# Optimization experiments

Measured on AMD Instinct MI355X. Metric: run time of the kernel, lower is better.

The kernel has to match this reference:

```python
import jax, jax.numpy as jnp
from jax import lax
import numpy as np

MAX_ITER = 12      # sifting iterations per IMF
TOL = 0.05         # sd tolerance / flatness tolerance
NUM_IMFS = 6       # max IMFs extracted
EPS = 1e-8


def _peak_mask(s):
    # strict local maxima, matching scipy.signal.find_peaks on plateau-free
    # (continuous random) signals: s[i-1] < s[i] > s[i+1]
    interior = (s[:, 1:-1] > s[:, :-2]) & (s[:, 1:-1] > s[:, 2:])
    return jnp.pad(interior, ((0, 0), (1, 1)))  # [B, L] bool


def _interp_env(s, mask):
    # piecewise-linear interpolation through masked peaks, flat extrapolation
    # at the ends (np.interp with left=first peak val, right=last peak val)
    B, L = s.shape
    idx = jnp.arange(L)
    last = lax.cummax(jnp.where(mask, idx, -1), axis=1)               # prev peak idx (-1 if none)
    nxt = lax.cummin(jnp.where(mask, idx, L), axis=1, reverse=True)   # next peak idx (L if none)
    vl = jnp.take_along_axis(s, jnp.clip(last, 0, L - 1), axis=1)
    vr = jnp.take_along_axis(s, jnp.clip(nxt, 0, L - 1), axis=1)
    denom = nxt - last
    frac = jnp.where(denom > 0,
                     (idx - last).astype(s.dtype) / jnp.maximum(denom, 1).astype(s.dtype),
                     jnp.zeros((), s.dtype))
    env = vl + frac * (vr - vl)
    env = jnp.where(last < 0, vr, env)   # left of first peak
    env = jnp.where(nxt >= L, vl, env)   # right of last peak
    return env


def _envelope(s, upper):
    mask = _peak_mask(s) if upper else _peak_mask(-s)
    env = _interp_env(s, mask)
    # fallback when fewer than 2 peaks: running max / running min of s
    fb = lax.cummax(s, axis=1) if upper else lax.cummin(s, axis=1)
    few = mask.sum(axis=1, keepdims=True) < 2
    return jnp.where(few, fb, env)


def _extract_imf(signal):
    # iterative sifting with early-stop masked into a fixed-length scan
    def body(carry, _):
        h, done = carry
        mean = 0.5 * (_envelope(h, True) + _envelope(h, False))
        # sd = sum((h - h_new)^2) / (sum(h^2)+eps) and h - h_new == mean
        sd = jnp.sum(mean ** 2) / (jnp.sum(h ** 2) + EPS)
        conv = sd < TOL
        h_next = jnp.where(done | conv, h, h - mean)
        return (h_next, done | conv), None
    (h, _), _ = lax.scan(body, (signal, jnp.array(False)), None, length=MAX_ITER)
    return h, signal - h


def _emd(x):
    def step(carry, _):
        res, done = carry
        imf, new_res = _extract_imf(res)
        imf = jnp.where(done, jnp.zeros_like(imf), imf)
        new_res = jnp.where(done, res, new_res)
        # _is_residual_flat: var(diff) < tol * var(residual) (torch.var unbiased)
        d = jnp.diff(new_res, axis=-1)
        flat = jnp.var(d, ddof=1) < TOL * jnp.var(new_res, ddof=1)
        return (new_res, done | flat), imf
    (res, _), imfs = lax.scan(step, (x, jnp.array(False)), None, length=NUM_IMFS)
    # stack IMFs and residual: [NUM_IMFS+1, B, L]; IMFs after early stop are zeros
    return jnp.concatenate([imfs, res[None]], axis=0)


def setup_inputs() -> dict:
    key = jax.random.key(0)
    x = jax.random.normal(key, (64, 16384), dtype=jnp.float32)
    return {"x": x}


def reference(x):
    return _emd(x)
```

## Files before the change

kernel.cpp:

```cpp
#include <hip/hip_runtime.h>

#define NL 16384
#define NB 64
#define NT 1024
#define NC (NL / NT)
#define NW (NT / 64)
#define N_ITER 12
#define N_IMFS 6

#pragma clang fp contract(off)

#define HSZ (NL + (NL >> 5))
__device__ __forceinline__ int physi(int i) { return i + (i >> 5); }

#define FMAXV 3.402823466e38f

__global__ __launch_bounds__(NT, 4) void emd_main(
    const float* __restrict__ x, float* __restrict__ out,
    unsigned* cnt, double* sdsl, double* flsl) {
  __shared__ float hbuf[2 * HSZ];
  __shared__ int wLU[NW], wLL[NW], wNU[NW], wNL[NW];
  __shared__ float wMx[NW], wMn[NW];
  __shared__ unsigned wCT[NW];
  __shared__ int eLU[NW], eLL[NW], eNU[NW], eNL[NW];
  __shared__ float eMx[NW], eMn[NW];
  __shared__ unsigned sTot;
  __shared__ double tA[NW], tB[NW], tC[NW], tD[NW];
  __shared__ int sFlag;

  const int t = threadIdx.x;
  const int lane = t & 63;
  const int wv = t >> 6;
  const int row = blockIdx.x;
  const int base = t * NC;
  const float* xr = x + (size_t)row * NL;
  float* res = out + (size_t)N_IMFS * NB * NL + (size_t)row * NL;

  int off = 0;

  #pragma unroll
  for (int q = 0; q < NC / 4; q++) {
    int i0 = base + q * 4;
    float4 v = *(const float4*)&xr[i0];
    *(float4*)&hbuf[physi(i0)] = v;
    *(float4*)&res[i0] = v;
  }
  __syncthreads();

  unsigned ep = 0;
  bool done = false;

  for (int k = 0; k < N_IMFS; k++) {
    float* outk = out + (size_t)k * NB * NL + (size_t)row * NL;
    if (done) {
      #pragma unroll
      for (int q = 0; q < NC / 4; q++)
        *(float4*)&outk[base + q * 4] = make_float4(0.f, 0.f, 0.f, 0.f);
      continue;
    }

    for (int it = 0; it < N_ITER; it++) {
      float* hcur = hbuf + off;
      float* hnx  = hbuf + (off ^ HSZ);

      unsigned mU = 0, mL = 0;
      int lmU = -1, lmL = -1, cU = 0, cL = 0;
      float rmx = -FMAXV, rmn = FMAXV;
      {
        float hm = (base > 0) ? hcur[physi(base - 1)] : 0.0f;
        float4 cur = *(const float4*)&hcur[physi(base)];
        #define PKSTEP(J, HC, HP) { int i = base + (J);                     \
          bool in = (i > 0) && (i + 1 < NL);                                \
          if (in && hm < (HC) && (HC) > (HP)) { mU |= 1u << (J); lmU = i; cU++; } \
          if (in && hm > (HC) && (HC) < (HP)) { mL |= 1u << (J); lmL = i; cL++; } \
          rmx = fmaxf(rmx, (HC)); rmn = fminf(rmn, (HC)); hm = (HC); }
        #pragma unroll
        for (int q = 0; q < 4; q++) {
          float4 nxt = cur;
          float n0;
          if (q < 3) { nxt = *(const float4*)&hcur[physi(base + q * 4 + 4)]; n0 = nxt.x; }
          else       { n0 = (base + 16 < NL) ? hcur[physi(base + 16)] : 0.0f; }
          PKSTEP(q * 4 + 0, cur.x, cur.y)
          PKSTEP(q * 4 + 1, cur.y, cur.z)
          PKSTEP(q * 4 + 2, cur.z, cur.w)
          PKSTEP(q * 4 + 3, cur.w, n0)
          cur = nxt;
        }
        #undef PKSTEP
      }
      int fpU = mU ? (base + __ffs(mU) - 1) : NL;
      int fpL = mL ? (base + __ffs(mL) - 1) : NL;
      unsigned long long bUm = __ballot(mU != 0);
      unsigned long long bLm = __ballot(mL != 0);
      {
        int s;
        s = bUm ? (63 - __clzll((long long)bUm)) : 0;
        if (lane == s) wLU[wv] = bUm ? lmU : -1;
        s = bLm ? (63 - __clzll((long long)bLm)) : 0;
        if (lane == s) wLL[wv] = bLm ? lmL : -1;
        s = bUm ? (__ffsll(bUm) - 1) : 0;
        if (lane == s) wNU[wv] = bUm ? fpU : NL;
        s = bLm ? (__ffsll(bLm) - 1) : 0;
        if (lane == s) wNL[wv] = bLm ? fpL : NL;
      }
      unsigned ict = ((unsigned)cU << 16) | (unsigned)cL;
      #pragma unroll
      for (int o = 1; o < 64; o <<= 1) {
        unsigned cc = __shfl_down(ict, o, 64);
        if (lane + o < 64) ict += cc;
      }
      if (lane == 0) wCT[wv] = ict;
      __syncthreads();
      if (t == 0) {
        int aLU = -1, aLL = -1; unsigned tt = 0;
        for (int w = 0; w < NW; w++) {
          eLU[w] = aLU; aLU = max(aLU, wLU[w]);
          eLL[w] = aLL; aLL = max(aLL, wLL[w]);
          tt += wCT[w];
        }
        int aNU = NL, aNL = NL;
        for (int w = NW - 1; w >= 0; w--) {
          eNU[w] = aNU; aNU = min(aNU, wNU[w]);
          eNL[w] = aNL; aNL = min(aNL, wNL[w]);
        }
        sTot = tt;
      }
      __syncthreads();
      const unsigned tot = sTot;
      const int totU = (int)(tot >> 16), totL = (int)(tot & 0xffffu);

      unsigned long long belowU = bUm & ((1ull << lane) - 1ull);
      unsigned long long belowL = bLm & ((1ull << lane) - 1ull);
      unsigned long long aboveU = (lane == 63) ? 0ull : (bUm & (~0ull << (lane + 1)));
      unsigned long long aboveL = (lane == 63) ? 0ull : (bLm & (~0ull << (lane + 1)));
      int slU = belowU ? (63 - __clzll((long long)belowU)) : 0;
      int slL = belowL ? (63 - __clzll((long long)belowL)) : 0;
      int snU = aboveU ? (__ffsll(aboveU) - 1) : 0;
      int snL = aboveL ? (__ffsll(aboveL) - 1) : 0;
      int gU  = __shfl(lmU, slU, 64);
      int gL  = __shfl(lmL, slL, 64);
      int gNU = __shfl(fpU, snU, 64);
      int gNL = __shfl(fpL, snL, 64);
      const int clU = belowU ? gU  : eLU[wv];
      const int clL = belowL ? gL  : eLL[wv];
      const int cnU = aboveU ? gNU : eNU[wv];
      const int cnL = aboveL ? gNL : eNL[wv];

      float crx = -FMAXV, crn = FMAXV;
      if (totU < 2 || totL < 2) {
        float iMx = rmx, iMn = rmn;
        #pragma unroll
        for (int o = 1; o < 64; o <<= 1) {
          float fa = __shfl_up(iMx, o, 64);
          float fb = __shfl_up(iMn, o, 64);
          if (lane >= o) { iMx = fmaxf(iMx, fa); iMn = fminf(iMn, fb); }
        }
        if (lane == 63) { wMx[wv] = iMx; wMn[wv] = iMn; }
        __syncthreads();
        if (t == 0) {
          float aMx = -FMAXV, aMn = FMAXV;
          for (int w = 0; w < NW; w++) {
            eMx[w] = aMx; aMx = fmaxf(aMx, wMx[w]);
            eMn[w] = aMn; aMn = fminf(aMn, wMn[w]);
          }
        }
        __syncthreads();
        float pMx = __shfl_up(iMx, 1, 64); if (lane == 0) pMx = -FMAXV;
        float pMn = __shfl_up(iMn, 1, 64); if (lane == 0) pMn = FMAXV;
        crx = fmaxf(eMx[wv], pMx);
        crn = fminf(eMn[wv], pMn);
      }

      double pm2 = 0.0, ph2 = 0.0;
      {
        float rx = crx, rn = crn;
        int curLU = clU, curLL = clL;
        float vl = hcur[physi(clU < 0 ? 0 : clU)];
        float wl = hcur[physi(clL < 0 ? 0 : clL)];
        int gB = -0x7fffffff, gD = -0x7fffffff;
        float vr = 0.0f, wr = 0.0f;
        #define ENVSTEP(J, HC, OD) { int i = base + (J); float hc = (HC);   \
          rx = fmaxf(rx, hc); rn = fminf(rn, hc);                           \
          if ((mU >> (J)) & 1u) { curLU = i; vl = hc; }                     \
          if ((mL >> (J)) & 1u) { curLL = i; wl = hc; }                     \
          int lU = curLU, lL = curLL;                                       \
          unsigned highm = 0xFFFFFFFFu << (J); unsigned a;                  \
          a = mU & highm; int nUv = a ? (base + __ffs(a) - 1) : cnU;        \
          a = mL & highm; int nLv = a ? (base + __ffs(a) - 1) : cnL;        \
          if (nUv != gB) { gB = nUv; vr = hcur[physi(nUv >= NL ? NL - 1 : nUv)]; } \
          if (nLv != gD) { gD = nLv; wr = hcur[physi(nLv >= NL ? NL - 1 : nLv)]; } \
          int den = nUv - lU;                                               \
          float fracU = (float)(i - lU) / (float)(den > 0 ? den : 1);       \
          float envU = (den > 0) ? __builtin_fmaf(fracU, vr - vl, vl) : vl; \
          if (lU < 0) envU = vr;                                            \
          if (nUv >= NL) envU = vl;                                         \
          if (totU < 2) envU = rx;                                          \
          int den2 = nLv - lL;                                              \
          float fracL = (float)(i - lL) / (float)(den2 > 0 ? den2 : 1);     \
          float envL = (den2 > 0) ? __builtin_fmaf(fracL, wr - wl, wl) : wl;\
          if (lL < 0) envL = wr;                                            \
          if (nLv >= NL) envL = wl;                                         \
          if (totL < 2) envL = rn;                                          \
          float mn = 0.5f * (envU + envL);                                  \
          (OD) = hc - mn;                                                   \
          pm2 += (double)mn * (double)mn; ph2 += (double)hc * (double)hc; }
        #pragma unroll
        for (int q = 0; q < 4; q++) {
          int i0 = base + q * 4;
          float4 hv4 = *(const float4*)&hcur[physi(i0)];
          float4 o4;
          ENVSTEP(q * 4 + 0, hv4.x, o4.x)
          ENVSTEP(q * 4 + 1, hv4.y, o4.y)
          ENVSTEP(q * 4 + 2, hv4.z, o4.z)
          ENVSTEP(q * 4 + 3, hv4.w, o4.w)
          *(float4*)&hnx[physi(i0)] = o4;
        }
        #undef ENVSTEP
      }
      #pragma unroll
      for (int o = 1; o < 64; o <<= 1) {
        double a = __shfl_down(pm2, o, 64);
        double b = __shfl_down(ph2, o, 64);
        if (lane + o < 64) { pm2 += a; ph2 += b; }
      }
      if (lane == 0) { tA[wv] = pm2; tB[wv] = ph2; }
      ep++;
      __syncthreads();
      if (t == 0) {
        double sA = 0.0, sB = 0.0;
        for (int w = 0; w < NW; w++) { sA += tA[w]; sB += tB[w]; }
        atomicAdd(&sdsl[(k * N_ITER + it) * 2 + 0], sA);
        atomicAdd(&sdsl[(k * N_ITER + it) * 2 + 1], sB);
        __hip_atomic_fetch_add(cnt, 1u, __ATOMIC_ACQ_REL, __HIP_MEMORY_SCOPE_AGENT);
        unsigned tgt = ep * gridDim.x;
        while (__hip_atomic_load(cnt, __ATOMIC_ACQUIRE, __HIP_MEMORY_SCOPE_AGENT) < tgt)
          __builtin_amdgcn_s_sleep(1);
        double m2 = __hip_atomic_load(&sdsl[(k * N_ITER + it) * 2 + 0],
                                      __ATOMIC_RELAXED, __HIP_MEMORY_SCOPE_AGENT);
        double h2 = __hip_atomic_load(&sdsl[(k * N_ITER + it) * 2 + 1],
                                      __ATOMIC_RELAXED, __HIP_MEMORY_SCOPE_AGENT);
        sFlag = (m2 / (h2 + 1e-8) < 0.05) ? 1 : 0;
      }
      __syncthreads();
      if (sFlag) break;
      off ^= HSZ;
    }

    float* hcur = hbuf + off;
    double s1 = 0.0, s2 = 0.0, s3 = 0.0, s4 = 0.0;
    {
      float rb = 0.0f;
      if (base + NC < NL) rb = res[base + NC] - hcur[physi(base + NC)];
      float4 rv4 = *(const float4*)&res[base];
      float4 hv4 = *(const float4*)&hcur[physi(base)];
      float e0 = rv4.x - hv4.x, e1 = rv4.y - hv4.y,
            e2 = rv4.z - hv4.z, e3 = rv4.w - hv4.w;
      #define FLSTEP(J, CUR, NXT) { int i = base + (J);                     \
        s1 += (double)(CUR); s2 += (double)(CUR) * (double)(CUR);           \
        if (i + 1 < NL) { float dd = (NXT) - (CUR);                         \
          s3 += (double)dd; s4 += (double)dd * (double)dd; } }
      #pragma unroll
      for (int q = 0; q < 4; q++) {
        float c0 = e0, c1 = e1, c2 = e2, c3 = e3;
        float n0;
        if (q < 3) {
          int i0 = base + q * 4 + 4;
          rv4 = *(const float4*)&res[i0];
          hv4 = *(const float4*)&hcur[physi(i0)];
          e0 = rv4.x - hv4.x; e1 = rv4.y - hv4.y;
          e2 = rv4.z - hv4.z; e3 = rv4.w - hv4.w;
          n0 = e0;
        } else n0 = rb;
        FLSTEP(q * 4 + 0, c0, c1)
        FLSTEP(q * 4 + 1, c1, c2)
        FLSTEP(q * 4 + 2, c2, c3)
        FLSTEP(q * 4 + 3, c3, n0)
      }
      #undef FLSTEP
    }
    #pragma unroll
    for (int o = 1; o < 64; o <<= 1) {
      double a = __shfl_down(s1, o, 64);
      double b = __shfl_down(s2, o, 64);
      double c = __shfl_down(s3, o, 64);
      double d = __shfl_down(s4, o, 64);
      if (lane + o < 64) { s1 += a; s2 += b; s3 += c; s4 += d; }
    }
    if (lane == 0) { tA[wv] = s1; tB[wv] = s2; tC[wv] = s3; tD[wv] = s4; }
    __syncthreads();
    if (t == 0) {
      double S1 = 0.0, S2 = 0.0, S3 = 0.0, S4 = 0.0;
      for (int w = 0; w < NW; w++) { S1 += tA[w]; S2 += tB[w]; S3 += tC[w]; S4 += tD[w]; }
      atomicAdd(&flsl[k * 4 + 0], S1);
      atomicAdd(&flsl[k * 4 + 1], S2);
      atomicAdd(&flsl[k * 4 + 2], S3);
      atomicAdd(&flsl[k * 4 + 3], S4);
    }
    #pragma unroll
    for (int q = 0; q < NC / 4; q++) {
      int i0 = base + q * 4;
      int p0 = physi(i0);
      float4 rv = *(const float4*)&res[i0];
      float4 hv = *(const float4*)&hcur[p0];
      float4 rq = make_float4(rv.x - hv.x, rv.y - hv.y, rv.z - hv.z, rv.w - hv.w);
      *(float4*)&outk[i0] = hv;
      *(float4*)&res[i0] = rq;
      *(float4*)&hcur[p0] = rq;
    }
    ep++;
    __syncthreads();
    if (t == 0) {
      __hip_atomic_fetch_add(cnt, 1u, __ATOMIC_ACQ_REL, __HIP_MEMORY_SCOPE_AGENT);
      unsigned tgt = ep * gridDim.x;
      while (__hip_atomic_load(cnt, __ATOMIC_ACQUIRE, __HIP_MEMORY_SCOPE_AGENT) < tgt)
        __builtin_amdgcn_s_sleep(1);
      double S1 = __hip_atomic_load(&flsl[k * 4 + 0], __ATOMIC_RELAXED, __HIP_MEMORY_SCOPE_AGENT);
      double S2 = __hip_atomic_load(&flsl[k * 4 + 1], __ATOMIC_RELAXED, __HIP_MEMORY_SCOPE_AGENT);
      double S3 = __hip_atomic_load(&flsl[k * 4 + 2], __ATOMIC_RELAXED, __HIP_MEMORY_SCOPE_AGENT);
      double S4 = __hip_atomic_load(&flsl[k * 4 + 3], __ATOMIC_RELAXED, __HIP_MEMORY_SCOPE_AGENT);
      double nr = (double)NB * (double)NL;
      double nd = (double)NB * (double)(NL - 1);
      double varr = (S2 - S1 * S1 / nr) / (nr - 1.0);
      double vard = (S4 - S3 * S3 / nd) / (nd - 1.0);
      sFlag = (vard < 0.05 * varr) ? 1 : 0;
    }
    __syncthreads();
    done = done || (sFlag != 0);
  }
}

extern "C" void kernel_launch(void* const* d_in, const int* in_sizes, int n_in,
                              void* d_out, int out_size, void* d_ws, size_t ws_size,
                              hipStream_t stream) {
  const float* x = (const float*)d_in[0];
  float* out = (float*)d_out;
  size_t zb = ws_size < 4096 ? ws_size : 4096;
  hipMemsetAsync(d_ws, 0, zb, stream);
  unsigned* cnt = (unsigned*)d_ws;
  double* sdsl = (double*)((char*)d_ws + 256);
  double* flsl = (double*)((char*)d_ws + 256 + (size_t)N_IMFS * N_ITER * 2 * 8);
  hipLaunchKernelGGL(emd_main, dim3(NB), dim3(NT), 0, stream, x, out, cnt, sdsl, flsl);
}
```

Before: 286.2 us.

## Split each row across four cooperating blocks with global boundary exchange

Each signal row is now handled by four blocks, one per quarter-segment, so the grid grows from 64 to 256 blocks and each thread owns 4 samples instead of 16. Blocks of the same row trade boundary samples, per-segment peak summaries and running max/min through workspace memory, and wait on a per-row atomic counter barrier every sifting iteration. The aim is to occupy more compute units, since 64 blocks leave most of the GPU idle. The cost is an extra inter-block spin barrier and global-memory round trips on every iteration.

```diff
diff --git a/kernel.cpp b/kernel.cpp
--- a/kernel.cpp
+++ b/kernel.cpp
@@ -2,94 +2,124 @@
 
 #define NL 16384
 #define NB 64
+#define NSEG 4
+#define SEG (NL / NSEG)
 #define NT 1024
-#define NC (NL / NT)
+#define NC (SEG / NT)
 #define NW (NT / 64)
 #define N_ITER 12
 #define N_IMFS 6
 
 #pragma clang fp contract(off)
 
-#define HSZ (NL + (NL >> 5))
+#define HSZS (SEG + (SEG >> 5))
 __device__ __forceinline__ int physi(int i) { return i + (i >> 5); }
 
 #define FMAXV 3.402823466e38f
 
+__device__ __forceinline__ void gstore(float* p, float v) {
+  __hip_atomic_store(p, v, __ATOMIC_RELAXED, __HIP_MEMORY_SCOPE_AGENT);
+}
+__device__ __forceinline__ float gload(float* p) {
+  return __hip_atomic_load(p, __ATOMIC_RELAXED, __HIP_MEMORY_SCOPE_AGENT);
+}
+
 __global__ __launch_bounds__(NT, 4) void emd_main(
-    const float* __restrict__ x, float* __restrict__ out,
-    unsigned* cnt, double* sdsl, double* flsl) {
-  __shared__ float hbuf[2 * HSZ];
+    const float* __restrict__ x, float* __restrict__ out, char* __restrict__ ws) {
+  unsigned* cnt    = (unsigned*)ws;
+  double*   sdsl   = (double*)(ws + 256);
+  double*   flsl   = (double*)(ws + 1408);
+  unsigned* rowcnt = (unsigned*)(ws + 2048);
+  float*    hbg    = (float*)(ws + 6144);
+  float*    bsm    = (float*)(ws + 10240);
+  float*    rsb    = (float*)(ws + 26624);
+
+  __shared__ float hbuf[2 * HSZS];
   __shared__ int wLU[NW], wLL[NW], wNU[NW], wNL[NW];
   __shared__ float wMx[NW], wMn[NW];
   __shared__ unsigned wCT[NW];
   __shared__ int eLU[NW], eLL[NW], eNU[NW], eNL[NW];
+  __shared__ float eLUv[NW], eLLv[NW], eNUv[NW], eNLv[NW];
   __shared__ float eMx[NW], eMn[NW];
+  __shared__ float bsl[12];
+  __shared__ float nbs[NSEG][12];
   __shared__ unsigned sTot;
+  __shared__ float sBMx, sBMn;
   __shared__ double tA[NW], tB[NW], tC[NW], tD[NW];
   __shared__ int sFlag;
 
   const int t = threadIdx.x;
   const int lane = t & 63;
   const int wv = t >> 6;
-  const int row = blockIdx.x;
-  const int base = t * NC;
+  const int bid = blockIdx.x;
+  const int row = bid >> 2;
+  const int seg = bid & 3;
+  const int seg0 = seg * SEG;
+  const int seg1 = seg0 + SEG;
+  const int bl = t * NC;
+  const int bg = seg0 + bl;
   const float* xr = x + (size_t)row * NL;
   float* res = out + (size_t)N_IMFS * NB * NL + (size_t)row * NL;
 
   int off = 0;
-
-  #pragma unroll
-  for (int q = 0; q < NC / 4; q++) {
-    int i0 = base + q * 4;
-    float4 v = *(const float4*)&xr[i0];
-    *(float4*)&hbuf[physi(i0)] = v;
-    *(float4*)&res[i0] = v;
+  int hb = 0;
+  unsigned ep = 0;
+  unsigned rep = 0;
+
+  {
+    float4 v = *(const float4*)&xr[bg];
+    *(float4*)&hbuf[physi(bl)] = v;
+    *(float4*)&res[bg] = v;
+    if (t == 0) { gstore(&hbg[(0 * 256 + bid) * 2 + 0], v.x); gstore(&rsb[bid], v.x); }
+    if (t == NT - 1) gstore(&hbg[(0 * 256 + bid) * 2 + 1], v.w);
   }
   __syncthreads();
-
-  unsigned ep = 0;
+  rep++;
+  if (t == 0) {
+    __hip_atomic_fetch_add(&rowcnt[row * 16], 1u, __ATOMIC_ACQ_REL, __HIP_MEMORY_SCOPE_AGENT);
+    while (__hip_atomic_load(&rowcnt[row * 16], __ATOMIC_ACQUIRE, __HIP_MEMORY_SCOPE_AGENT) < rep * NSEG)
+      __builtin_amdgcn_s_sleep(1);
+  }
+  __syncthreads();
+
   bool done = false;
 
   for (int k = 0; k < N_IMFS; k++) {
     float* outk = out + (size_t)k * NB * NL + (size_t)row * NL;
     if (done) {
-      #pragma unroll
-      for (int q = 0; q < NC / 4; q++)
-        *(float4*)&outk[base + q * 4] = make_float4(0.f, 0.f, 0.f, 0.f);
+      *(float4*)&outk[bg] = make_float4(0.f, 0.f, 0.f, 0.f);
       continue;
     }
 
     for (int it = 0; it < N_ITER; it++) {
       float* hcur = hbuf + off;
-      float* hnx  = hbuf + (off ^ HSZ);
+      float* hnx  = hbuf + (off ^ HSZS);
 
       unsigned mU = 0, mL = 0;
       int lmU = -1, lmL = -1, cU = 0, cL = 0;
       float rmx = -FMAXV, rmn = FMAXV;
       {
-        float hm = (base > 0) ? hcur[physi(base - 1)] : 0.0f;
-        float4 cur = *(const float4*)&hcur[physi(base)];
-        #define PKSTEP(J, HC, HP) { int i = base + (J);                     \
-          bool in = (i > 0) && (i + 1 < NL);                                \
+        float hbPrev = 0.0f, hbNext = 0.0f;
+        if (bl == 0 && bg > 0)
+          hbPrev = gload(&hbg[(hb * 256 + bid - 1) * 2 + 1]);
+        if (bl + NC == SEG && bg + NC < NL)
+          hbNext = gload(&hbg[(hb * 256 + bid + 1) * 2 + 0]);
+        float hm = (bg > 0) ? ((bl > 0) ? hcur[physi(bl - 1)] : hbPrev) : 0.0f;
+        float nextv = (bl + NC < SEG) ? hcur[physi(bl + NC)] : hbNext;
+        float4 cur = *(const float4*)&hcur[physi(bl)];
+        #define PKSTEP(J, HC, HP) { int i = bg + (J);                         \
+          bool in = (i > 0) && (i + 1 < NL);                                  \
           if (in && hm < (HC) && (HC) > (HP)) { mU |= 1u << (J); lmU = i; cU++; } \
           if (in && hm > (HC) && (HC) < (HP)) { mL |= 1u << (J); lmL = i; cL++; } \
           rmx = fmaxf(rmx, (HC)); rmn = fminf(rmn, (HC)); hm = (HC); }
-        #pragma unroll
-        for (int q = 0; q < 4; q++) {
-          float4 nxt = cur;
-          float n0;
-          if (q < 3) { nxt = *(const float4*)&hcur[physi(base + q * 4 + 4)]; n0 = nxt.x; }
-          else       { n0 = (base + 16 < NL) ? hcur[physi(base + 16)] : 0.0f; }
-          PKSTEP(q * 4 + 0, cur.x, cur.y)
-          PKSTEP(q * 4 + 1, cur.y, cur.z)
-          PKSTEP(q * 4 + 2, cur.z, cur.w)
-          PKSTEP(q * 4 + 3, cur.w, n0)
-          cur = nxt;
-        }
+        PKSTEP(0, cur.x, cur.y)
+        PKSTEP(1, cur.y, cur.z)
+        PKSTEP(2, cur.z, cur.w)
+        PKSTEP(3, cur.w, nextv)
         #undef PKSTEP
       }
-      int fpU = mU ? (base + __ffs(mU) - 1) : NL;
-      int fpL = mL ? (base + __ffs(mL) - 1) : NL;
+      int fpU = mU ? (bg + __ffs(mU) - 1) : NL;
+      int fpL = mL ? (bg + __ffs(mL) - 1) : NL;
       unsigned long long bUm = __ballot(mU != 0);
       unsigned long long bLm = __ballot(mL != 0);
       {
@@ -104,26 +134,89 @@
         if (lane == s) wNL[wv] = bLm ? fpL : NL;
       }
       unsigned ict = ((unsigned)cU << 16) | (unsigned)cL;
-      #pragma unroll
-      for (int o = 1; o < 64; o <<= 1) {
-        unsigned cc = __shfl_down(ict, o, 64);
-        if (lane + o < 64) ict += cc;
-      }
-      if (lane == 0) wCT[wv] = ict;
+      {
+        float wmx = rmx, wmn = rmn;
+        #pragma unroll
+        for (int o = 1; o < 64; o <<= 1) {
+          unsigned cc = __shfl_down(ict, o, 64);
+          float fa = __shfl_down(wmx, o, 64);
+          float fb = __shfl_down(wmn, o, 64);
+          if (lane + o < 64) { ict += cc; wmx = fmaxf(wmx, fa); wmn = fminf(wmn, fb); }
+        }
+        if (lane == 0) { wCT[wv] = ict; wMx[wv] = wmx; wMn[wv] = wmn; }
+      }
       __syncthreads();
       if (t == 0) {
-        int aLU = -1, aLL = -1; unsigned tt = 0;
+        int aLU = -1, aLL = -1, aNU = NL, aNL = NL;
+        float aMx = -FMAXV, aMn = FMAXV; unsigned tt = 0;
         for (int w = 0; w < NW; w++) {
-          eLU[w] = aLU; aLU = max(aLU, wLU[w]);
-          eLL[w] = aLL; aLL = max(aLL, wLL[w]);
+          if (wLU[w] > aLU) aLU = wLU[w];
+          if (wLL[w] > aLL) aLL = wLL[w];
+          if (wNU[w] < aNU) aNU = wNU[w];
+          if (wNL[w] < aNL) aNL = wNL[w];
+          aMx = fmaxf(aMx, wMx[w]); aMn = fminf(aMn, wMn[w]);
           tt += wCT[w];
         }
-        int aNU = NL, aNL = NL;
+        bsl[0] = __int_as_float(aLU);
+        bsl[1] = (aLU >= 0) ? hcur[physi(aLU - seg0)] : 0.0f;
+        bsl[2] = __int_as_float(aLL);
+        bsl[3] = (aLL >= 0) ? hcur[physi(aLL - seg0)] : 0.0f;
+        bsl[4] = __int_as_float(aNU);
+        bsl[5] = (aNU < NL) ? hcur[physi(aNU - seg0)] : 0.0f;
+        bsl[6] = __int_as_float(aNL);
+        bsl[7] = (aNL < NL) ? hcur[physi(aNL - seg0)] : 0.0f;
+        bsl[8] = aMx; bsl[9] = aMn;
+        bsl[10] = __uint_as_float(tt);
+        bsl[11] = 0.f;
+      }
+      __syncthreads();
+      rep++;
+      if (wv == 0) {
+        if (lane < 12) gstore(&bsm[bid * 16 + lane], bsl[lane]);
+        if (lane == 0) {
+          __hip_atomic_fetch_add(&rowcnt[row * 16], 1u, __ATOMIC_ACQ_REL, __HIP_MEMORY_SCOPE_AGENT);
+          while (__hip_atomic_load(&rowcnt[row * 16], __ATOMIC_ACQUIRE, __HIP_MEMORY_SCOPE_AGENT) < rep * NSEG)
+            __builtin_amdgcn_s_sleep(1);
+        }
+        if (lane < 48) {
+          int s = lane / 12, sl = lane % 12;
+          nbs[s][sl] = gload(&bsm[(row * 4 + s) * 16 + sl]);
+        }
+      }
+      __syncthreads();
+      if (t == 0) {
+        int bclU = -1, bclL = -1; float bclUv = 0.f, bclLv = 0.f;
+        float bMx = -FMAXV, bMn = FMAXV;
+        for (int s = 0; s < seg; s++) {
+          int v = __float_as_int(nbs[s][0]);
+          if (v > bclU) { bclU = v; bclUv = nbs[s][1]; }
+          v = __float_as_int(nbs[s][2]);
+          if (v > bclL) { bclL = v; bclLv = nbs[s][3]; }
+          bMx = fmaxf(bMx, nbs[s][8]);
+          bMn = fminf(bMn, nbs[s][9]);
+        }
+        int bcnU = NL, bcnL = NL; float bcnUv = 0.f, bcnLv = 0.f;
+        for (int s = NSEG - 1; s > seg; s--) {
+          int v = __float_as_int(nbs[s][4]);
+          if (v < bcnU) { bcnU = v; bcnUv = nbs[s][5]; }
+          v = __float_as_int(nbs[s][6]);
+          if (v < bcnL) { bcnL = v; bcnLv = nbs[s][7]; }
+        }
+        unsigned tot = 0;
+        for (int s = 0; s < NSEG; s++) tot += __float_as_uint(nbs[s][10]);
+        sTot = tot; sBMx = bMx; sBMn = bMn;
+        int aLU = bclU, aLL = bclL; float aLUv = bclUv, aLLv = bclLv;
+        for (int w = 0; w < NW; w++) {
+          eLU[w] = aLU; eLUv[w] = aLUv; eLL[w] = aLL; eLLv[w] = aLLv;
+          if (wLU[w] > aLU) { aLU = wLU[w]; aLUv = hcur[physi(aLU - seg0)]; }
+          if (wLL[w] > aLL) { aLL = wLL[w]; aLLv = hcur[physi(aLL - seg0)]; }
+        }
+        int aNU = bcnU, aNL2 = bcnL; float aNUv = bcnUv, aNLv = bcnLv;
         for (int w = NW - 1; w >= 0; w--) {
-          eNU[w] = aNU; aNU = min(aNU, wNU[w]);
-          eNL[w] = aNL; aNL = min(aNL, wNL[w]);
-        }
-        sTot = tt;
+          eNU[w] = aNU; eNUv[w] = aNUv; eNL[w] = aNL2; eNLv[w] = aNLv;
+          if (wNU[w] < aNU) { aNU = wNU[w]; aNUv = hcur[physi(aNU - seg0)]; }
+          if (wNL[w] < aNL2) { aNL2 = wNL[w]; aNLv = hcur[physi(aNL2 - seg0)]; }
+        }
       }
       __syncthreads();
       const unsigned tot = sTot;
@@ -145,6 +238,10 @@
       const int clL = belowL ? gL  : eLL[wv];
       const int cnU = aboveU ? gNU : eNU[wv];
       const int cnL = aboveL ? gNL : eNL[wv];
+      const float cnUv = eNUv[wv];
+      const float cnLv = eNLv[wv];
+      float vl0 = belowU ? hcur[physi(gU - seg0)] : ((clU >= 0) ? eLUv[wv] : 0.0f);
+      float wl0 = belowL ? hcur[physi(gL - seg0)] : ((clL >= 0) ? eLLv[wv] : 0.0f);
 
       float crx = -FMAXV, crn = FMAXV;
       if (totU < 2 || totL < 2) {
@@ -158,7 +255,7 @@
         if (lane == 63) { wMx[wv] = iMx; wMn[wv] = iMn; }
         __syncthreads();
         if (t == 0) {
-          float aMx = -FMAXV, aMn = FMAXV;
+          float aMx = sBMx, aMn = sBMn;
           for (int w = 0; w < NW; w++) {
             eMx[w] = aMx; aMx = fmaxf(aMx, wMx[w]);
             eMn[w] = aMn; aMn = fminf(aMn, wMn[w]);
@@ -175,47 +272,47 @@
       {
         float rx = crx, rn = crn;
         int curLU = clU, curLL = clL;
-        float vl = hcur[physi(clU < 0 ? 0 : clU)];
-        float wl = hcur[physi(clL < 0 ? 0 : clL)];
+        float vl = vl0, wl = wl0;
         int gB = -0x7fffffff, gD = -0x7fffffff;
         float vr = 0.0f, wr = 0.0f;
-        #define ENVSTEP(J, HC, OD) { int i = base + (J); float hc = (HC);   \
-          rx = fmaxf(rx, hc); rn = fminf(rn, hc);                           \
-          if ((mU >> (J)) & 1u) { curLU = i; vl = hc; }                     \
-          if ((mL >> (J)) & 1u) { curLL = i; wl = hc; }                     \
-          int lU = curLU, lL = curLL;                                       \
-          unsigned highm = 0xFFFFFFFFu << (J); unsigned a;                  \
-          a = mU & highm; int nUv = a ? (base + __ffs(a) - 1) : cnU;        \
-          a = mL & highm; int nLv = a ? (base + __ffs(a) - 1) : cnL;        \
-          if (nUv != gB) { gB = nUv; vr = hcur[physi(nUv >= NL ? NL - 1 : nUv)]; } \
-          if (nLv != gD) { gD = nLv; wr = hcur[physi(nLv >= NL ? NL - 1 : nLv)]; } \
-          int den = nUv - lU;                                               \
-          float fracU = (float)(i - lU) / (float)(den > 0 ? den : 1);       \
-          float envU = (den > 0) ? __builtin_fmaf(fracU, vr - vl, vl) : vl; \
-          if (lU < 0) envU = vr;                                            \
-          if (nUv >= NL) envU = vl;                                         \
-          if (totU < 2) envU = rx;                                          \
-          int den2 = nLv - lL;                                              \
-          float fracL = (float)(i - lL) / (float)(den2 > 0 ? den2 : 1);     \
-          float envL = (den2 > 0) ? __builtin_fmaf(fracL, wr - wl, wl) : wl;\
-          if (lL < 0) envL = wr;                                            \
-          if (nLv >= NL) envL = wl;                                         \
-          if (totL < 2) envL = rn;                                          \
-          float mn = 0.5f * (envU + envL);                                  \
-          (OD) = hc - mn;                                                   \
+        #define ENVSTEP(J, HC, OD) { int i = bg + (J); float hc = (HC);       \
+          rx = fmaxf(rx, hc); rn = fminf(rn, hc);                             \
+          if ((mU >> (J)) & 1u) { curLU = i; vl = hc; }                       \
+          if ((mL >> (J)) & 1u) { curLL = i; wl = hc; }                       \
+          int lU = curLU, lL = curLL;                                         \
+          unsigned highm = 0xFFFFFFFFu << (J); unsigned a;                    \
+          a = mU & highm; int nUv = a ? (bg + __ffs(a) - 1) : cnU;            \
+          a = mL & highm; int nLv = a ? (bg + __ffs(a) - 1) : cnL;            \
+          if (nUv != gB) { gB = nUv;                                          \
+            vr = (nUv < seg1) ? hcur[physi(nUv - seg0)] : cnUv; }             \
+          if (nLv != gD) { gD = nLv;                                          \
+            wr = (nLv < seg1) ? hcur[physi(nLv - seg0)] : cnLv; }             \
+          int den = nUv - lU;                                                 \
+          float fracU = (float)(i - lU) / (float)(den > 0 ? den : 1);         \
+          float envU = (den > 0) ? __builtin_fmaf(fracU, vr - vl, vl) : vl;   \
+          if (lU < 0) envU = vr;                                              \
+          if (nUv >= NL) envU = vl;                                           \
+          if (totU < 2) envU = rx;                                            \
+          int den2 = nLv - lL;                                                \
+          float fracL = (float)(i - lL) / (float)(den2 > 0 ? den2 : 1);       \
+          float envL = (den2 > 0) ? __builtin_fmaf(fracL, wr - wl, wl) : wl;  \
+          if (lL < 0) envL = wr;                                              \
+          if (nLv >= NL) envL = wl;                                           \
+          if (totL < 2) envL = rn;                                            \
+          float mn = 0.5f * (envU + envL);                                    \
+          (OD) = hc - mn;                                                     \
           pm2 += (double)mn * (double)mn; ph2 += (double)hc * (double)hc; }
-        #pragma unroll
-        for (int q = 0; q < 4; q++) {
-          int i0 = base + q * 4;
-          float4 hv4 = *(const float4*)&hcur[physi(i0)];
-          float4 o4;
-          ENVSTEP(q * 4 + 0, hv4.x, o4.x)
-          ENVSTEP(q * 4 + 1, hv4.y, o4.y)
-          ENVSTEP(q * 4 + 2, hv4.z, o4.z)
-          ENVSTEP(q * 4 + 3, hv4.w, o4.w)
-          *(float4*)&hnx[physi(i0)] = o4;
-        }
+        float4 hv4 = *(const float4*)&hcur[physi(bl)];
+        float4 o4;
+        ENVSTEP(0, hv4.x, o4.x)
+        ENVSTEP(1, hv4.y, o4.y)
+        ENVSTEP(2, hv4.z, o4.z)
+        ENVSTEP(3, hv4.w, o4.w)
         #undef ENVSTEP
+        *(float4*)&hnx[physi(bl)] = o4;
+        int nhb = hb ^ 1;
+        if (t == 0)      gstore(&hbg[(nhb * 256 + bid) * 2 + 0], o4.x);
+        if (t == NT - 1) gstore(&hbg[(nhb * 256 + bid) * 2 + 1], o4.w);
       }
       #pragma unroll
       for (int o = 1; o < 64; o <<= 1) {
@@ -243,39 +340,31 @@
       }
       __syncthreads();
       if (sFlag) break;
-      off ^= HSZ;
+      off ^= HSZS; hb ^= 1;
     }
 
     float* hcur = hbuf + off;
     double s1 = 0.0, s2 = 0.0, s3 = 0.0, s4 = 0.0;
     {
-      float rb = 0.0f;
-      if (base + NC < NL) rb = res[base + NC] - hcur[physi(base + NC)];
-      float4 rv4 = *(const float4*)&res[base];
-      float4 hv4 = *(const float4*)&hcur[physi(base)];
+      float rbv = 0.0f;
+      if (bg + NC < NL) {
+        float rnext = (bl + NC < SEG) ? res[bg + NC] : gload(&rsb[bid + 1]);
+        float hnext = (bl + NC < SEG) ? hcur[physi(bl + NC)]
+                                      : gload(&hbg[(hb * 256 + bid + 1) * 2 + 0]);
+        rbv = rnext - hnext;
+      }
+      float4 rv4 = *(const float4*)&res[bg];
+      float4 hv4 = *(const float4*)&hcur[physi(bl)];
       float e0 = rv4.x - hv4.x, e1 = rv4.y - hv4.y,
             e2 = rv4.z - hv4.z, e3 = rv4.w - hv4.w;
-      #define FLSTEP(J, CUR, NXT) { int i = base + (J);                     \
-        s1 += (double)(CUR); s2 += (double)(CUR) * (double)(CUR);           \
-        if (i + 1 < NL) { float dd = (NXT) - (CUR);                         \
+      #define FLSTEP(J, CUR, NXT) { int i = bg + (J);                         \
+        s1 += (double)(CUR); s2 += (double)(CUR) * (double)(CUR);             \
+        if (i + 1 < NL) { float dd = (NXT) - (CUR);                           \
           s3 += (double)dd; s4 += (double)dd * (double)dd; } }
-      #pragma unroll
-      for (int q = 0; q < 4; q++) {
-        float c0 = e0, c1 = e1, c2 = e2, c3 = e3;
-        float n0;
-        if (q < 3) {
-          int i0 = base + q * 4 + 4;
-          rv4 = *(const float4*)&res[i0];
-          hv4 = *(const float4*)&hcur[physi(i0)];
-          e0 = rv4.x - hv4.x; e1 = rv4.y - hv4.y;
-          e2 = rv4.z - hv4.z; e3 = rv4.w - hv4.w;
-          n0 = e0;
-        } else n0 = rb;
-        FLSTEP(q * 4 + 0, c0, c1)
-        FLSTEP(q * 4 + 1, c1, c2)
-        FLSTEP(q * 4 + 2, c2, c3)
-        FLSTEP(q * 4 + 3, c3, n0)
-      }
+      FLSTEP(0, e0, e1)
+      FLSTEP(1, e1, e2)
+      FLSTEP(2, e2, e3)
+      FLSTEP(3, e3, rbv)
       #undef FLSTEP
     }
     #pragma unroll
@@ -296,16 +385,19 @@
       atomicAdd(&flsl[k * 4 + 2], S3);
       atomicAdd(&flsl[k * 4 + 3], S4);
     }
-    #pragma unroll
-    for (int q = 0; q < NC / 4; q++) {
-      int i0 = base + q * 4;
-      int p0 = physi(i0);
-      float4 rv = *(const float4*)&res[i0];
-      float4 hv = *(const float4*)&hcur[p0];
-      float4 rq = make_float4(rv.x - hv.x, rv.y - hv.y, rv.z - hv.z, rv.w - hv.w);
-      *(float4*)&outk[i0] = hv;
-      *(float4*)&res[i0] = rq;
-      *(float4*)&hcur[p0] = rq;
+    {
+      float4 rv4 = *(const float4*)&res[bg];
+      float4 hv4 = *(const float4*)&hcur[physi(bl)];
+      float4 rq = make_float4(rv4.x - hv4.x, rv4.y - hv4.y,
+                              rv4.z - hv4.z, rv4.w - hv4.w);
+      *(float4*)&outk[bg] = hv4;
+      *(float4*)&res[bg] = rq;
+      *(float4*)&hcur[physi(bl)] = rq;
+      if (t == 0) {
+        gstore(&hbg[(hb * 256 + bid) * 2 + 0], rq.x);
+        gstore(&rsb[bid], rq.x);
+      }
+      if (t == NT - 1) gstore(&hbg[(hb * 256 + bid) * 2 + 1], rq.w);
     }
     ep++;
     __syncthreads();
@@ -334,10 +426,8 @@
                               hipStream_t stream) {
   const float* x = (const float*)d_in[0];
   float* out = (float*)d_out;
-  size_t zb = ws_size < 4096 ? ws_size : 4096;
+  size_t zb = ws_size < 6144 ? ws_size : 6144;
   hipMemsetAsync(d_ws, 0, zb, stream);
-  unsigned* cnt = (unsigned*)d_ws;
-  double* sdsl = (double*)((char*)d_ws + 256);
-  double* flsl = (double*)((char*)d_ws + 256 + (size_t)N_IMFS * N_ITER * 2 * 8);
-  hipLaunchKernelGGL(emd_main, dim3(NB), dim3(NT), 0, stream, x, out, cnt, sdsl, flsl);
+  hipLaunchKernelGGL(emd_main, dim3(NB * NSEG), dim3(NT), 0, stream,
+                     x, out, (char*)d_ws);
 }
```

After: 448.1 us. +56.6%, slower.

## Speculatively overlap grid-wide convergence checks with the next sifting iteration

Applied to the files above, without the earlier changes.

Swaps the blocking grid barrier after each sifting iteration and each IMF for per-slot arrival counters. Each block publishes its partial sums, runs the next iteration speculatively, and only waits on the previous slot's counter at the start of the following iteration, rolling back the buffer swap if convergence had been reached. The flatness check is deferred in the same way, so one IMF's residual update overlaps the other blocks' reductions. This hides cross-block barrier latency, at the cost of possibly wasted speculative work and more delicate buffer-parity logic.

```diff
diff --git a/kernel.cpp b/kernel.cpp
--- a/kernel.cpp
+++ b/kernel.cpp
@@ -16,8 +16,12 @@
 #define FMAXV 3.402823466e38f
 
 __global__ __launch_bounds__(NT, 4) void emd_main(
-    const float* __restrict__ x, float* __restrict__ out,
-    unsigned* cnt, double* sdsl, double* flsl) {
+    const float* __restrict__ x, float* __restrict__ out, char* __restrict__ ws) {
+  unsigned* scnt = (unsigned*)ws;
+  double*   sdsl = (double*)(ws + 512);
+  unsigned* fcnt = (unsigned*)(ws + 2048);
+  double*   flsl = (double*)(ws + 2304);
+
   __shared__ float hbuf[2 * HSZ];
   __shared__ int wLU[NW], wLL[NW], wNU[NW], wNL[NW];
   __shared__ float wMx[NW], wMn[NW];
@@ -47,7 +51,6 @@
   }
   __syncthreads();
 
-  unsigned ep = 0;
   bool done = false;
 
   for (int k = 0; k < N_IMFS; k++) {
@@ -59,7 +62,20 @@
       continue;
     }
 
+    int fin = 0;
     for (int it = 0; it < N_ITER; it++) {
+      if (it >= 1) {
+        if (t == 0) {
+          int s = k * N_ITER + (it - 1);
+          while (__hip_atomic_load(&scnt[s], __ATOMIC_ACQUIRE, __HIP_MEMORY_SCOPE_AGENT) < NB)
+            __builtin_amdgcn_s_sleep(1);
+          double m2 = __hip_atomic_load(&sdsl[s * 2 + 0], __ATOMIC_RELAXED, __HIP_MEMORY_SCOPE_AGENT);
+          double h2 = __hip_atomic_load(&sdsl[s * 2 + 1], __ATOMIC_RELAXED, __HIP_MEMORY_SCOPE_AGENT);
+          sFlag = (m2 / (h2 + 1e-8) < 0.05) ? 1 : 0;
+        }
+        __syncthreads();
+        if (sFlag) { off ^= HSZ; fin = 1; break; }
+      }
       float* hcur = hbuf + off;
       float* hnx  = hbuf + (off ^ HSZ);
 
@@ -224,29 +240,56 @@
         if (lane + o < 64) { pm2 += a; ph2 += b; }
       }
       if (lane == 0) { tA[wv] = pm2; tB[wv] = ph2; }
-      ep++;
       __syncthreads();
       if (t == 0) {
         double sA = 0.0, sB = 0.0;
         for (int w = 0; w < NW; w++) { sA += tA[w]; sB += tB[w]; }
-        atomicAdd(&sdsl[(k * N_ITER + it) * 2 + 0], sA);
-        atomicAdd(&sdsl[(k * N_ITER + it) * 2 + 1], sB);
-        __hip_atomic_fetch_add(cnt, 1u, __ATOMIC_ACQ_REL, __HIP_MEMORY_SCOPE_AGENT);
-        unsigned tgt = ep * gridDim.x;
-        while (__hip_atomic_load(cnt, __ATOMIC_ACQUIRE, __HIP_MEMORY_SCOPE_AGENT) < tgt)
+        int s = k * N_ITER + it;
+        atomicAdd(&sdsl[s * 2 + 0], sA);
+        atomicAdd(&sdsl[s * 2 + 1], sB);
+        __hip_atomic_fetch_add(&scnt[s], 1u, __ATOMIC_ACQ_REL, __HIP_MEMORY_SCOPE_AGENT);
+      }
+      off ^= HSZ;
+    }
+    if (!fin) {
+      if (t == 0) {
+        int s = k * N_ITER + (N_ITER - 1);
+        while (__hip_atomic_load(&scnt[s], __ATOMIC_ACQUIRE, __HIP_MEMORY_SCOPE_AGENT) < NB)
           __builtin_amdgcn_s_sleep(1);
-        double m2 = __hip_atomic_load(&sdsl[(k * N_ITER + it) * 2 + 0],
-                                      __ATOMIC_RELAXED, __HIP_MEMORY_SCOPE_AGENT);
-        double h2 = __hip_atomic_load(&sdsl[(k * N_ITER + it) * 2 + 1],
-                                      __ATOMIC_RELAXED, __HIP_MEMORY_SCOPE_AGENT);
+        double m2 = __hip_atomic_load(&sdsl[s * 2 + 0], __ATOMIC_RELAXED, __HIP_MEMORY_SCOPE_AGENT);
+        double h2 = __hip_atomic_load(&sdsl[s * 2 + 1], __ATOMIC_RELAXED, __HIP_MEMORY_SCOPE_AGENT);
         sFlag = (m2 / (h2 + 1e-8) < 0.05) ? 1 : 0;
       }
       __syncthreads();
-      if (sFlag) break;
-      off ^= HSZ;
+      if (sFlag) off ^= HSZ;
     }
 
     float* hcur = hbuf + off;
+
+    if (k > 0) {
+      if (t == 0) {
+        while (__hip_atomic_load(&fcnt[k - 1], __ATOMIC_ACQUIRE, __HIP_MEMORY_SCOPE_AGENT) < NB)
+          __builtin_amdgcn_s_sleep(1);
+        double S1 = __hip_atomic_load(&flsl[(k - 1) * 4 + 0], __ATOMIC_RELAXED, __HIP_MEMORY_SCOPE_AGENT);
+        double S2 = __hip_atomic_load(&flsl[(k - 1) * 4 + 1], __ATOMIC_RELAXED, __HIP_MEMORY_SCOPE_AGENT);
+        double S3 = __hip_atomic_load(&flsl[(k - 1) * 4 + 2], __ATOMIC_RELAXED, __HIP_MEMORY_SCOPE_AGENT);
+        double S4 = __hip_atomic_load(&flsl[(k - 1) * 4 + 3], __ATOMIC_RELAXED, __HIP_MEMORY_SCOPE_AGENT);
+        double nr = (double)NB * (double)NL;
+        double nd = (double)NB * (double)(NL - 1);
+        double varr = (S2 - S1 * S1 / nr) / (nr - 1.0);
+        double vard = (S4 - S3 * S3 / nd) / (nd - 1.0);
+        sFlag = (vard < 0.05 * varr) ? 1 : 0;
+      }
+      __syncthreads();
+      if (sFlag) done = true;
+    }
+    if (done) {
+      #pragma unroll
+      for (int q = 0; q < NC / 4; q++)
+        *(float4*)&outk[base + q * 4] = make_float4(0.f, 0.f, 0.f, 0.f);
+      continue;
+    }
+
     double s1 = 0.0, s2 = 0.0, s3 = 0.0, s4 = 0.0;
     {
       float rb = 0.0f;
@@ -295,6 +338,7 @@
       atomicAdd(&flsl[k * 4 + 1], S2);
       atomicAdd(&flsl[k * 4 + 2], S3);
       atomicAdd(&flsl[k * 4 + 3], S4);
+      __hip_atomic_fetch_add(&fcnt[k], 1u, __ATOMIC_ACQ_REL, __HIP_MEMORY_SCOPE_AGENT);
     }
     #pragma unroll
     for (int q = 0; q < NC / 4; q++) {
@@ -307,25 +351,7 @@
       *(float4*)&res[i0] = rq;
       *(float4*)&hcur[p0] = rq;
     }
-    ep++;
     __syncthreads();
-    if (t == 0) {
-      __hip_atomic_fetch_add(cnt, 1u, __ATOMIC_ACQ_REL, __HIP_MEMORY_SCOPE_AGENT);
-      unsigned tgt = ep * gridDim.x;
-      while (__hip_atomic_load(cnt, __ATOMIC_ACQUIRE, __HIP_MEMORY_SCOPE_AGENT) < tgt)
-        __builtin_amdgcn_s_sleep(1);
-      double S1 = __hip_atomic_load(&flsl[k * 4 + 0], __ATOMIC_RELAXED, __HIP_MEMORY_SCOPE_AGENT);
-      double S2 = __hip_atomic_load(&flsl[k * 4 + 1], __ATOMIC_RELAXED, __HIP_MEMORY_SCOPE_AGENT);
-      double S3 = __hip_atomic_load(&flsl[k * 4 + 2], __ATOMIC_RELAXED, __HIP_MEMORY_SCOPE_AGENT);
-      double S4 = __hip_atomic_load(&flsl[k * 4 + 3], __ATOMIC_RELAXED, __HIP_MEMORY_SCOPE_AGENT);
-      double nr = (double)NB * (double)NL;
-      double nd = (double)NB * (double)(NL - 1);
-      double varr = (S2 - S1 * S1 / nr) / (nr - 1.0);
-      double vard = (S4 - S3 * S3 / nd) / (nd - 1.0);
-      sFlag = (vard < 0.05 * varr) ? 1 : 0;
-    }
-    __syncthreads();
-    done = done || (sFlag != 0);
   }
 }
 
@@ -336,8 +362,6 @@
   float* out = (float*)d_out;
   size_t zb = ws_size < 4096 ? ws_size : 4096;
   hipMemsetAsync(d_ws, 0, zb, stream);
-  unsigned* cnt = (unsigned*)d_ws;
-  double* sdsl = (double*)((char*)d_ws + 256);
-  double* flsl = (double*)((char*)d_ws + 256 + (size_t)N_IMFS * N_ITER * 2 * 8);
-  hipLaunchKernelGGL(emd_main, dim3(NB), dim3(NT), 0, stream, x, out, cnt, sdsl, flsl);
+  hipLaunchKernelGGL(emd_main, dim3(NB), dim3(NT), 0, stream,
+                     x, out, (char*)d_ws);
 }
```

Measured after the change: 330.6 us. 15.5% more time.
